# Kernel tuning notes

Hardware: AMD Instinct MI355X
Metric: run time of the kernel (lower is better)

The kernel has to match this reference:

```python
import jax, jax.numpy as jnp
import numpy as np

D_MODEL = 1024
NUM_HEADS = 16
NUM_KV_HEADS = 4
HEAD_DIM = D_MODEL // NUM_HEADS  # 64
THETA = 10000.0
MAX_SEQ_LEN = 4096


def _rope_tables(max_seq_len, d_k, theta):
    k_vec = jnp.arange(0, d_k, 2, dtype=jnp.float32) / d_k
    freq = 1.0 / (theta ** k_vec)                       # (d_k/2,)
    ang = jnp.arange(max_seq_len, dtype=jnp.float32)[:, None] * freq[None, :]
    return jnp.cos(ang), jnp.sin(ang)                   # each (max_seq_len, d_k/2)


def _apply_rope(x, pos, cos_table, sin_table):
    # x: (b, h, l, d), pos: (b, l)
    cos = cos_table[pos][:, None, :, :]                 # (b, 1, l, d/2)
    sin = sin_table[pos][:, None, :, :]
    even, odd = x[..., 0::2], x[..., 1::2]
    r1 = even * cos - odd * sin
    r2 = even * sin + odd * cos
    return jnp.stack([r1, r2], axis=-1).reshape(x.shape)  # interleave back


def setup_inputs() -> dict:
    key = jax.random.key(0)
    ks = jax.random.split(key, 6)
    B, L, D = 1, 4096, D_MODEL
    std = (2.0 / (D + D)) ** 0.5
    std_kv = (2.0 / (D + HEAD_DIM * NUM_KV_HEADS)) ** 0.5
    x = jax.random.normal(ks[0], (B, L, D), dtype=jnp.float32)
    Wq = jax.random.normal(ks[1], (D, D), dtype=jnp.float32) * std
    Wk = jax.random.normal(ks[2], (HEAD_DIM * NUM_KV_HEADS, D), dtype=jnp.float32) * std_kv
    Wv = jax.random.normal(ks[3], (HEAD_DIM * NUM_KV_HEADS, D), dtype=jnp.float32) * std_kv
    Wo = jax.random.normal(ks[4], (D, D), dtype=jnp.float32) * std
    token_positions = jnp.broadcast_to(jnp.arange(L, dtype=jnp.int32), (B, L))
    return {"x": x, "Wq": Wq, "Wk": Wk, "Wv": Wv, "Wo": Wo,
            "token_positions": token_positions}


def reference(x, Wq, Wk, Wv, Wo, token_positions):
    B, L, D = x.shape
    H, Hkv, Dh = NUM_HEADS, NUM_KV_HEADS, HEAD_DIM
    n_rep = H // Hkv
    cos_t, sin_t = _rope_tables(MAX_SEQ_LEN, Dh, THETA)

    q = (x @ Wq.T).reshape(B, L, H, Dh).transpose(0, 2, 1, 3)      # b h l d
    k = (x @ Wk.T).reshape(B, L, Hkv, Dh).transpose(0, 2, 1, 3)    # b g l d
    v = (x @ Wv.T).reshape(B, L, Hkv, Dh).transpose(0, 2, 1, 3)

    q = _apply_rope(q, token_positions, cos_t, sin_t)
    k = _apply_rope(k, token_positions, cos_t, sin_t)

    # GQA: group query heads by kv head
    qg = q.reshape(B, Hkv, n_rep, L, Dh)
    scores = jnp.einsum('bgrqd,bgkd->bgrqk', qg, k) / jnp.sqrt(jnp.float32(Dh))
    causal = jnp.tril(jnp.ones((L, L), dtype=bool))
    scores = jnp.where(causal, scores, -jnp.inf)
    weights = jax.nn.softmax(scores, axis=-1)
    out = jnp.einsum('bgrqk,bgkd->bgrqd', weights, v)              # b g r q d
    out = out.reshape(B, H, L, Dh).transpose(0, 2, 1, 3).reshape(B, L, D)
    return out @ Wo.T
```

## Files before the change

### kernel.cpp

```cpp
#include <hip/hip_runtime.h>
#include <hip/hip_bf16.h>
#include <math.h>

typedef __bf16 bf16;
typedef __bf16 v8bf __attribute__((ext_vector_type(8)));
typedef __bf16 v4bf __attribute__((ext_vector_type(4)));
typedef float f32x4 __attribute__((ext_vector_type(4)));

#define L_SEQ 4096
#define DMODEL 1024
#define NHEADS 16
#define DH 64
#define NEG_BIG (-1e30f)
#define LN1E4_64 0.14391156f

__global__ void convert_all(const float* __restrict__ x, const float* __restrict__ wq,
                            const float* __restrict__ wk, const float* __restrict__ wv,
                            const float* __restrict__ wo,
                            bf16* __restrict__ xb, bf16* __restrict__ wqkvb,
                            bf16* __restrict__ wob) {
    int i = (blockIdx.x * 256 + threadIdx.x) * 4;
    const float* src;
    bf16* dst;
    if (i < 4194304)      { src = x  + i;             dst = xb    + i; }
    else if (i < 5242880) { src = wq + (i - 4194304); dst = wqkvb + (i - 4194304); }
    else if (i < 5505024) { src = wk + (i - 5242880); dst = wqkvb + 1048576 + (i - 5242880); }
    else if (i < 5767168) { src = wv + (i - 5505024); dst = wqkvb + 1310720 + (i - 5505024); }
    else                  { src = wo + (i - 5767168); dst = wob   + (i - 5767168); }
    f32x4 v = *(const f32x4*)src;
    v4bf r;
#pragma unroll
    for (int j = 0; j < 4; j++) r[j] = (bf16)v[j];
    *(v4bf*)dst = r;
}

__global__ __launch_bounds__(512) void gemm_qkv(const bf16* __restrict__ A,
                                                const bf16* __restrict__ W,
                                                bf16* __restrict__ Qb,
                                                bf16* __restrict__ Kb,
                                                bf16* __restrict__ Vtg,
                                                const int* __restrict__ tp) {
    __shared__ bf16 As[128][68];
    __shared__ bf16 Bs[128][68];
    const int K = 1024;
    const int tid = threadIdx.x;
    const int w = tid >> 6, lane = tid & 63;
    const int quad = lane >> 4, l16 = lane & 15;
    const int wm = (w & 1) * 64, wn = (w >> 1) * 32;
    const int bm = blockIdx.y * 128, bn = blockIdx.x * 128;

    f32x4 acc[4][2];
#pragma unroll
    for (int mf = 0; mf < 4; mf++)
#pragma unroll
        for (int nf = 0; nf < 2; nf++) acc[mf][nf] = (f32x4){0.f, 0.f, 0.f, 0.f};

    const int sr = tid >> 2;
    const int scb = (tid & 3) * 16;

    v8bf pa0, pa1, pb0, pb1;
    {
        const bf16* ap = &A[(size_t)(bm + sr) * K + scb];
        const bf16* bp = &W[(size_t)(bn + sr) * K + scb];
        pa0 = *(const v8bf*)ap; pa1 = *(const v8bf*)(ap + 8);
        pb0 = *(const v8bf*)bp; pb1 = *(const v8bf*)(bp + 8);
        *(v8bf*)&As[sr][scb] = pa0; *(v8bf*)&As[sr][scb + 8] = pa1;
        *(v8bf*)&Bs[sr][scb] = pb0; *(v8bf*)&Bs[sr][scb + 8] = pb1;
    }

    for (int kt = 0; kt < K; kt += 64) {
        __syncthreads();
        const bool more = (kt + 64) < K;
        if (more) {
            const bf16* ap = &A[(size_t)(bm + sr) * K + kt + 64 + scb];
            const bf16* bp = &W[(size_t)(bn + sr) * K + kt + 64 + scb];
            pa0 = *(const v8bf*)ap; pa1 = *(const v8bf*)(ap + 8);
            pb0 = *(const v8bf*)bp; pb1 = *(const v8bf*)(bp + 8);
        }
#pragma unroll
        for (int kf = 0; kf < 2; kf++) {
            v8bf a[4], b[2];
#pragma unroll
            for (int mf = 0; mf < 4; mf++) a[mf] = *(v8bf*)&As[wm + mf * 16 + l16][kf * 32 + quad * 8];
#pragma unroll
            for (int nf = 0; nf < 2; nf++) b[nf] = *(v8bf*)&Bs[wn + nf * 16 + l16][kf * 32 + quad * 8];
#pragma unroll
            for (int mf = 0; mf < 4; mf++)
#pragma unroll
                for (int nf = 0; nf < 2; nf++)
                    acc[mf][nf] = __builtin_amdgcn_mfma_f32_16x16x32_bf16(a[mf], b[nf], acc[mf][nf], 0, 0, 0);
        }
        __syncthreads();
        if (more) {
            *(v8bf*)&As[sr][scb] = pa0; *(v8bf*)&As[sr][scb + 8] = pa1;
            *(v8bf*)&Bs[sr][scb] = pb0; *(v8bf*)&Bs[sr][scb + 8] = pb1;
        }
    }

    if (bn < 1024) {
#pragma unroll
        for (int mf = 0; mf < 4; mf++) {
            int pos_[4];
#pragma unroll
            for (int r = 0; r < 4; r++) pos_[r] = tp[bm + wm + mf * 16 + quad * 4 + r];
#pragma unroll
            for (int nf = 0; nf < 2; nf++) {
                const int col = bn + wn + nf * 16 + l16;
                float fr = __expf(-(float)((col & 63) & ~1) * LN1E4_64);
#pragma unroll
                for (int r = 0; r < 4; r++) {
                    float v = acc[mf][nf][r];
                    float sn, cs;
                    __sincosf((float)pos_[r] * fr, &sn, &cs);
                    float p = __shfl_xor(v, 1);
                    float res = (l16 & 1) ? (p * sn + v * cs) : (v * cs - p * sn);
                    int row = bm + wm + mf * 16 + quad * 4 + r;
                    Qb[(size_t)row * DMODEL + col] = (bf16)res;
                }
            }
        }
    } else if (bn < 1280) {
#pragma unroll
        for (int mf = 0; mf < 4; mf++) {
            int pos_[4];
#pragma unroll
            for (int r = 0; r < 4; r++) pos_[r] = tp[bm + wm + mf * 16 + quad * 4 + r];
#pragma unroll
            for (int nf = 0; nf < 2; nf++) {
                const int kcol = bn - 1024 + wn + nf * 16 + l16;
                float fr = __expf(-(float)((kcol & 63) & ~1) * LN1E4_64);
#pragma unroll
                for (int r = 0; r < 4; r++) {
                    float v = acc[mf][nf][r];
                    float sn, cs;
                    __sincosf((float)pos_[r] * fr, &sn, &cs);
                    float p = __shfl_xor(v, 1);
                    float res = (l16 & 1) ? (p * sn + v * cs) : (v * cs - p * sn);
                    int row = bm + wm + mf * 16 + quad * 4 + r;
                    Kb[(size_t)row * 256 + kcol] = (bf16)res;
                }
            }
        }
    } else {
#pragma unroll
        for (int mf = 0; mf < 4; mf++)
#pragma unroll
            for (int nf = 0; nf < 2; nf++) {
                v4bf pk;
#pragma unroll
                for (int r = 0; r < 4; r++) pk[r] = (bf16)acc[mf][nf][r];
                int vcol = bn - 1280 + wn + nf * 16 + l16;
                int row = bm + wm + mf * 16 + quad * 4;
                *(v4bf*)&Vtg[(size_t)vcol * L_SEQ + row] = pk;
            }
    }
}

__global__ __launch_bounds__(512) void gemm_out(const bf16* __restrict__ A,
                                                const bf16* __restrict__ W,
                                                float* __restrict__ C) {
    __shared__ bf16 As[128][68];
    __shared__ bf16 Bs[128][68];
    const int K = 1024, N = 1024;
    const int tid = threadIdx.x;
    const int w = tid >> 6, lane = tid & 63;
    const int quad = lane >> 4, l16 = lane & 15;
    const int wm = (w & 1) * 64, wn = (w >> 1) * 32;
    const int bm = blockIdx.y * 128, bn = blockIdx.x * 128;

    f32x4 acc[4][2];
#pragma unroll
    for (int mf = 0; mf < 4; mf++)
#pragma unroll
        for (int nf = 0; nf < 2; nf++) acc[mf][nf] = (f32x4){0.f, 0.f, 0.f, 0.f};

    const int sr = tid >> 2;
    const int scb = (tid & 3) * 16;

    v8bf pa0, pa1, pb0, pb1;
    {
        const bf16* ap = &A[(size_t)(bm + sr) * K + scb];
        const bf16* bp = &W[(size_t)(bn + sr) * K + scb];
        pa0 = *(const v8bf*)ap; pa1 = *(const v8bf*)(ap + 8);
        pb0 = *(const v8bf*)bp; pb1 = *(const v8bf*)(bp + 8);
        *(v8bf*)&As[sr][scb] = pa0; *(v8bf*)&As[sr][scb + 8] = pa1;
        *(v8bf*)&Bs[sr][scb] = pb0; *(v8bf*)&Bs[sr][scb + 8] = pb1;
    }

    for (int kt = 0; kt < K; kt += 64) {
        __syncthreads();
        const bool more = (kt + 64) < K;
        if (more) {
            const bf16* ap = &A[(size_t)(bm + sr) * K + kt + 64 + scb];
            const bf16* bp = &W[(size_t)(bn + sr) * K + kt + 64 + scb];
            pa0 = *(const v8bf*)ap; pa1 = *(const v8bf*)(ap + 8);
            pb0 = *(const v8bf*)bp; pb1 = *(const v8bf*)(bp + 8);
        }
#pragma unroll
        for (int kf = 0; kf < 2; kf++) {
            v8bf a[4], b[2];
#pragma unroll
            for (int mf = 0; mf < 4; mf++) a[mf] = *(v8bf*)&As[wm + mf * 16 + l16][kf * 32 + quad * 8];
#pragma unroll
            for (int nf = 0; nf < 2; nf++) b[nf] = *(v8bf*)&Bs[wn + nf * 16 + l16][kf * 32 + quad * 8];
#pragma unroll
            for (int mf = 0; mf < 4; mf++)
#pragma unroll
                for (int nf = 0; nf < 2; nf++)
                    acc[mf][nf] = __builtin_amdgcn_mfma_f32_16x16x32_bf16(a[mf], b[nf], acc[mf][nf], 0, 0, 0);
        }
        __syncthreads();
        if (more) {
            *(v8bf*)&As[sr][scb] = pa0; *(v8bf*)&As[sr][scb + 8] = pa1;
            *(v8bf*)&Bs[sr][scb] = pb0; *(v8bf*)&Bs[sr][scb + 8] = pb1;
        }
    }
#pragma unroll
    for (int mf = 0; mf < 4; mf++)
#pragma unroll
        for (int nf = 0; nf < 2; nf++)
#pragma unroll
            for (int r = 0; r < 4; r++) {
                int row = bm + wm + mf * 16 + quad * 4 + r;
                int col = bn + wn + nf * 16 + l16;
                C[(size_t)row * N + col] = acc[mf][nf][r];
            }
}

__global__ __launch_bounds__(256, 2) void flash5(const bf16* __restrict__ Q,
                                                 const bf16* __restrict__ Kb,
                                                 const bf16* __restrict__ Vtg,
                                                 bf16* __restrict__ O0,
                                                 bf16* __restrict__ O1,
                                                 float* __restrict__ ML) {
    __shared__ bf16 Ks[128][68];
    __shared__ bf16 Vt[64][132];
    __shared__ bf16 Ps[128][68];
    const int h = blockIdx.y, kvh = h >> 2;
    const int bx = blockIdx.x;
    const int tid = threadIdx.x;
    const int w = tid >> 6, lane = tid & 63;
    const int quad = lane >> 4, l16 = lane & 15;
    const int krow = tid >> 1, kcb = (tid & 1) * 32;
    const int vr = tid >> 2, vcb = (tid & 3) * 32;
    const float scl = 0.125f;

    for (int p = 0; p < 2; p++) {
        const int qb = p ? (31 - bx) : bx;
        const int T = qb + 1;
        const int k0 = p ? ((T + 1) >> 1) : 0;
        const int k1 = p ? T : ((T + 1) >> 1);
        bf16* Op = p ? O1 : O0;
        float* mlp = ML + (size_t)(p * NHEADS + h) * L_SEQ * 2;

        if (k0 >= k1) {
            for (int i = tid; i < 128 * 64; i += 256) {
                int rr = i >> 6, cc = i & 63;
                Op[(size_t)(qb * 128 + rr) * DMODEL + h * DH + cc] = (bf16)0.f;
            }
            if (tid < 128) {
                mlp[(qb * 128 + tid) * 2 + 0] = NEG_BIG;
                mlp[(qb * 128 + tid) * 2 + 1] = 0.f;
            }
            continue;
        }

        v8bf qf[2][2];
#pragma unroll
        for (int mf = 0; mf < 2; mf++)
#pragma unroll
            for (int kf = 0; kf < 2; kf++)
                qf[mf][kf] = *(const v8bf*)&Q[(size_t)(qb * 128 + w * 32 + mf * 16 + l16) * DMODEL
                                              + h * DH + kf * 32 + quad * 8];

        f32x4 oacc[2][4];
#pragma unroll
        for (int mf = 0; mf < 2; mf++)
#pragma unroll
            for (int d = 0; d < 4; d++) oacc[mf][d] = (f32x4){0.f, 0.f, 0.f, 0.f};
        float m_i[2][4], l_i[2][4];
#pragma unroll
        for (int mf = 0; mf < 2; mf++)
#pragma unroll
            for (int r = 0; r < 4; r++) { m_i[mf][r] = NEG_BIG; l_i[mf][r] = 0.f; }

        v8bf kreg[4], vreg[4];
        {
            const bf16* ks = &Kb[(size_t)(k0 * 128 + krow) * 256 + kvh * DH + kcb];
            const bf16* vs = &Vtg[(size_t)(kvh * DH + vr) * L_SEQ + k0 * 128 + vcb];
#pragma unroll
            for (int u = 0; u < 4; u++) { kreg[u] = *(const v8bf*)&ks[8 * u]; vreg[u] = *(const v8bf*)&vs[8 * u]; }
            __syncthreads();
#pragma unroll
            for (int u = 0; u < 4; u++) { *(v8bf*)&Ks[krow][kcb + 8 * u] = kreg[u]; *(v8bf*)&Vt[vr][vcb + 8 * u] = vreg[u]; }
        }

        for (int kb = k0; kb < k1; kb++) {
            __syncthreads();
            if (kb + 1 < k1) {
                const bf16* ks = &Kb[(size_t)((kb + 1) * 128 + krow) * 256 + kvh * DH + kcb];
                const bf16* vs = &Vtg[(size_t)(kvh * DH + vr) * L_SEQ + (kb + 1) * 128 + vcb];
#pragma unroll
                for (int u = 0; u < 4; u++) { kreg[u] = *(const v8bf*)&ks[8 * u]; vreg[u] = *(const v8bf*)&vs[8 * u]; }
            }

            f32x4 s[2][8];
#pragma unroll
            for (int n = 0; n < 8; n++) {
                v8bf b0 = *(v8bf*)&Ks[n * 16 + l16][quad * 8];
                v8bf b1 = *(v8bf*)&Ks[n * 16 + l16][32 + quad * 8];
#pragma unroll
                for (int mf = 0; mf < 2; mf++) {
                    s[mf][n] = (f32x4){0.f, 0.f, 0.f, 0.f};
                    s[mf][n] = __builtin_amdgcn_mfma_f32_16x16x32_bf16(qf[mf][0], b0, s[mf][n], 0, 0, 0);
                    s[mf][n] = __builtin_amdgcn_mfma_f32_16x16x32_bf16(qf[mf][1], b1, s[mf][n], 0, 0, 0);
                }
            }

            if (kb == qb) {
#pragma unroll
                for (int mf = 0; mf < 2; mf++) {
                    int rbase = qb * 128 + w * 32 + mf * 16 + quad * 4;
#pragma unroll
                    for (int n = 0; n < 8; n++) {
                        int colg = kb * 128 + n * 16 + l16;
#pragma unroll
                        for (int r = 0; r < 4; r++)
                            s[mf][n][r] = (colg <= rbase + r) ? s[mf][n][r] * scl : NEG_BIG;
                    }
                }
            } else {
#pragma unroll
                for (int mf = 0; mf < 2; mf++)
#pragma unroll
                    for (int n = 0; n < 8; n++)
#pragma unroll
                        for (int r = 0; r < 4; r++) s[mf][n][r] *= scl;
            }

            float mx[2][4];
#pragma unroll
            for (int mf = 0; mf < 2; mf++)
#pragma unroll
                for (int r = 0; r < 4; r++) {
                    float m0 = s[mf][0][r];
#pragma unroll
                    for (int n = 1; n < 8; n++) m0 = fmaxf(m0, s[mf][n][r]);
                    mx[mf][r] = m0;
                }
#pragma unroll
            for (int off = 1; off < 16; off <<= 1)
#pragma unroll
                for (int mf = 0; mf < 2; mf++)
#pragma unroll
                    for (int r = 0; r < 4; r++)
                        mx[mf][r] = fmaxf(mx[mf][r], __shfl_xor(mx[mf][r], off));

            float alpha[2][4], mnew[2][4], rs[2][4];
#pragma unroll
            for (int mf = 0; mf < 2; mf++)
#pragma unroll
                for (int r = 0; r < 4; r++) {
                    mnew[mf][r]  = fmaxf(m_i[mf][r], mx[mf][r]);
                    alpha[mf][r] = __expf(m_i[mf][r] - mnew[mf][r]);
                    rs[mf][r] = 0.f;
                }
#pragma unroll
            for (int mf = 0; mf < 2; mf++)
#pragma unroll
                for (int n = 0; n < 8; n++)
#pragma unroll
                    for (int r = 0; r < 4; r++) {
                        float pv = __expf(s[mf][n][r] - mnew[mf][r]);
                        s[mf][n][r] = pv;
                        rs[mf][r] += pv;
                    }
#pragma unroll
            for (int off = 1; off < 16; off <<= 1)
#pragma unroll
                for (int mf = 0; mf < 2; mf++)
#pragma unroll
                    for (int r = 0; r < 4; r++) rs[mf][r] += __shfl_xor(rs[mf][r], off);
#pragma unroll
            for (int mf = 0; mf < 2; mf++)
#pragma unroll
                for (int r = 0; r < 4; r++) {
                    l_i[mf][r] = l_i[mf][r] * alpha[mf][r] + rs[mf][r];
                    m_i[mf][r] = mnew[mf][r];
                }
#pragma unroll
            for (int mf = 0; mf < 2; mf++)
#pragma unroll
                for (int d = 0; d < 4; d++)
#pragma unroll
                    for (int r = 0; r < 4; r++) oacc[mf][d][r] *= alpha[mf][r];

#pragma unroll
            for (int half = 0; half < 2; half++) {
#pragma unroll
                for (int mf = 0; mf < 2; mf++)
#pragma unroll
                    for (int n = 0; n < 4; n++)
#pragma unroll
                        for (int r = 0; r < 4; r++)
                            Ps[w * 32 + mf * 16 + quad * 4 + r][n * 16 + l16] =
                                (bf16)s[mf][half * 4 + n][r];
#pragma unroll
                for (int kf = 0; kf < 2; kf++) {
#pragma unroll
                    for (int mf = 0; mf < 2; mf++) {
                        v8bf pa = *(v8bf*)&Ps[w * 32 + mf * 16 + l16][kf * 32 + quad * 8];
#pragma unroll
                        for (int d = 0; d < 4; d++) {
                            v8bf vb = *(v8bf*)&Vt[d * 16 + l16][half * 64 + kf * 32 + quad * 8];
                            oacc[mf][d] = __builtin_amdgcn_mfma_f32_16x16x32_bf16(pa, vb, oacc[mf][d], 0, 0, 0);
                        }
                    }
                }
            }

            __syncthreads();
            if (kb + 1 < k1) {
#pragma unroll
                for (int u = 0; u < 4; u++) { *(v8bf*)&Ks[krow][kcb + 8 * u] = kreg[u]; *(v8bf*)&Vt[vr][vcb + 8 * u] = vreg[u]; }
            }
        }

#pragma unroll
        for (int mf = 0; mf < 2; mf++)
#pragma unroll
            for (int d = 0; d < 4; d++)
#pragma unroll
                for (int r = 0; r < 4; r++) {
                    int row = qb * 128 + w * 32 + mf * 16 + quad * 4 + r;
                    Op[(size_t)row * DMODEL + h * DH + d * 16 + l16] = (bf16)oacc[mf][d][r];
                }
        if (l16 == 0) {
#pragma unroll
            for (int mf = 0; mf < 2; mf++)
#pragma unroll
                for (int r = 0; r < 4; r++) {
                    int row = qb * 128 + w * 32 + mf * 16 + quad * 4 + r;
                    mlp[row * 2 + 0] = m_i[mf][r];
                    mlp[row * 2 + 1] = l_i[mf][r];
                }
        }
    }
}

__global__ void combine(const bf16* __restrict__ O0, const bf16* __restrict__ O1,
                        const float* __restrict__ ML, bf16* __restrict__ Attn) {
    int gid = blockIdx.x * 256 + threadIdx.x;
    int row = gid >> 8;
    int cg = (gid & 255) * 4;
    int h = cg >> 6;
    const float* ml0 = ML + ((size_t)h * L_SEQ + row) * 2;
    const float* ml1 = ML + ((size_t)(NHEADS + h) * L_SEQ + row) * 2;
    float m0 = ml0[0], l0 = ml0[1], m1 = ml1[0], l1 = ml1[1];
    float m = fmaxf(m0, m1);
    float a0 = __expf(m0 - m), a1 = __expf(m1 - m);
    float inv = 1.f / (a0 * l0 + a1 * l1);
    v4bf o0 = *(const v4bf*)&O0[(size_t)row * DMODEL + cg];
    v4bf o1 = *(const v4bf*)&O1[(size_t)row * DMODEL + cg];
    v4bf res;
#pragma unroll
    for (int j = 0; j < 4; j++)
        res[j] = (bf16)((a0 * (float)o0[j] + a1 * (float)o1[j]) * inv);
    *(v4bf*)&Attn[(size_t)row * DMODEL + cg] = res;
}

extern "C" void kernel_launch(void* const* d_in, const int* in_sizes, int n_in,
                              void* d_out, int out_size, void* d_ws, size_t ws_size,
                              hipStream_t stream) {
    const float* x  = (const float*)d_in[0];
    const float* Wq = (const float*)d_in[1];
    const float* Wk = (const float*)d_in[2];
    const float* Wv = (const float*)d_in[3];
    const float* Wo = (const float*)d_in[4];
    const int*   tp = (const int*)d_in[5];
    float* out = (float*)d_out;

    bf16*  xb    = (bf16*)d_ws;
    bf16*  wqkvb = xb    + 4194304;
    bf16*  wob   = wqkvb + 1572864;
    bf16*  Qb    = wob   + 1048576;
    bf16*  Kb    = Qb    + 4194304;
    bf16*  Vtg   = Kb    + 1048576;
    float* MLf   = (float*)(Vtg + 1048576);
    bf16*  Attn  = xb;
    bf16*  O0    = (bf16*)d_out;
    bf16*  O1    = O0 + 4194304;

    convert_all<<<6656, 256, 0, stream>>>(x, Wq, Wk, Wv, Wo, xb, wqkvb, wob);
    gemm_qkv<<<dim3(12, 32), 512, 0, stream>>>(xb, wqkvb, Qb, Kb, Vtg, tp);
    flash5<<<dim3(32, NHEADS), 256, 0, stream>>>(Qb, Kb, Vtg, O0, O1, MLf);
    combine<<<4096, 256, 0, stream>>>(O0, O1, MLf, Attn);
    gemm_out<<<dim3(8, 32), 512, 0, stream>>>(Attn, wob, out);
}
```

Baseline: 226.2 us.

## Split attention KV range four ways, fold softmax scale into Q, share LDS

The flash kernel now splits each query block's causal key range into four partitions instead of two, launching 64x16 blocks that each handle two partitions chosen to balance work. A four-way combine kernel merges the partial outputs. The softmax scale and log2(e) are folded into Q at the RoPE epilogue so the inner loop can use exp2 without a per-score multiply. K and P tiles share one LDS buffer, guarded by an extra barrier, and launch bounds are raised to 4 blocks per SM. The aim is more parallelism and occupancy, paid for with extra partial-output traffic, a larger combine step and one more sync per iteration.

```diff
diff --git a/kernel.cpp b/kernel.cpp
--- a/kernel.cpp
+++ b/kernel.cpp
@@ -13,6 +13,9 @@
 #define DH 64
 #define NEG_BIG (-1e30f)
 #define LN1E4_64 0.14391156f
+#define QSCALE 0.18033688f
+
+__device__ inline float fast_exp2(float x) { return __builtin_amdgcn_exp2f(x); }
 
 __global__ void convert_all(const float* __restrict__ x, const float* __restrict__ wq,
                             const float* __restrict__ wk, const float* __restrict__ wv,
@@ -115,7 +118,7 @@
                     float p = __shfl_xor(v, 1);
                     float res = (l16 & 1) ? (p * sn + v * cs) : (v * cs - p * sn);
                     int row = bm + wm + mf * 16 + quad * 4 + r;
-                    Qb[(size_t)row * DMODEL + col] = (bf16)res;
+                    Qb[(size_t)row * DMODEL + col] = (bf16)(res * QSCALE);
                 }
             }
         }
@@ -227,15 +230,16 @@
             }
 }
 
-__global__ __launch_bounds__(256, 2) void flash5(const bf16* __restrict__ Q,
+__global__ __launch_bounds__(256, 4) void flash6(const bf16* __restrict__ Q,
                                                  const bf16* __restrict__ Kb,
                                                  const bf16* __restrict__ Vtg,
                                                  bf16* __restrict__ O0,
                                                  bf16* __restrict__ O1,
+                                                 bf16* __restrict__ O2,
+                                                 bf16* __restrict__ O3,
                                                  float* __restrict__ ML) {
-    __shared__ bf16 Ks[128][68];
+    __shared__ bf16 KsPs[128][68];
     __shared__ bf16 Vt[64][132];
-    __shared__ bf16 Ps[128][68];
     const int h = blockIdx.y, kvh = h >> 2;
     const int bx = blockIdx.x;
     const int tid = threadIdx.x;
@@ -243,19 +247,22 @@
     const int quad = lane >> 4, l16 = lane & 15;
     const int krow = tid >> 1, kcb = (tid & 1) * 32;
     const int vr = tid >> 2, vcb = (tid & 3) * 32;
-    const float scl = 0.125f;
+    bf16* const Ops[4] = {O0, O1, O2, O3};
+
+    const int q0 = bx >> 1, i0 = bx & 1;
 
     for (int p = 0; p < 2; p++) {
-        const int qb = p ? (31 - bx) : bx;
+        const int qb = p ? (31 - q0) : q0;
+        const int j  = p ? (3 - i0) : i0;
         const int T = qb + 1;
-        const int k0 = p ? ((T + 1) >> 1) : 0;
-        const int k1 = p ? T : ((T + 1) >> 1);
-        bf16* Op = p ? O1 : O0;
-        float* mlp = ML + (size_t)(p * NHEADS + h) * L_SEQ * 2;
+        const int k0 = (j * T) >> 2;
+        const int k1 = ((j + 1) * T) >> 2;
+        bf16* Op = Ops[j];
+        float* mlp = ML + (size_t)(j * NHEADS + h) * L_SEQ * 2;
 
         if (k0 >= k1) {
-            for (int i = tid; i < 128 * 64; i += 256) {
-                int rr = i >> 6, cc = i & 63;
+            for (int idx = tid; idx < 128 * 64; idx += 256) {
+                int rr = idx >> 6, cc = idx & 63;
                 Op[(size_t)(qb * 128 + rr) * DMODEL + h * DH + cc] = (bf16)0.f;
             }
             if (tid < 128) {
@@ -292,7 +299,7 @@
             for (int u = 0; u < 4; u++) { kreg[u] = *(const v8bf*)&ks[8 * u]; vreg[u] = *(const v8bf*)&vs[8 * u]; }
             __syncthreads();
 #pragma unroll
-            for (int u = 0; u < 4; u++) { *(v8bf*)&Ks[krow][kcb + 8 * u] = kreg[u]; *(v8bf*)&Vt[vr][vcb + 8 * u] = vreg[u]; }
+            for (int u = 0; u < 4; u++) { *(v8bf*)&KsPs[krow][kcb + 8 * u] = kreg[u]; *(v8bf*)&Vt[vr][vcb + 8 * u] = vreg[u]; }
         }
 
         for (int kb = k0; kb < k1; kb++) {
@@ -307,8 +314,8 @@
             f32x4 s[2][8];
 #pragma unroll
             for (int n = 0; n < 8; n++) {
-                v8bf b0 = *(v8bf*)&Ks[n * 16 + l16][quad * 8];
-                v8bf b1 = *(v8bf*)&Ks[n * 16 + l16][32 + quad * 8];
+                v8bf b0 = *(v8bf*)&KsPs[n * 16 + l16][quad * 8];
+                v8bf b1 = *(v8bf*)&KsPs[n * 16 + l16][32 + quad * 8];
 #pragma unroll
                 for (int mf = 0; mf < 2; mf++) {
                     s[mf][n] = (f32x4){0.f, 0.f, 0.f, 0.f};
@@ -326,16 +333,9 @@
                         int colg = kb * 128 + n * 16 + l16;
 #pragma unroll
                         for (int r = 0; r < 4; r++)
-                            s[mf][n][r] = (colg <= rbase + r) ? s[mf][n][r] * scl : NEG_BIG;
+                            s[mf][n][r] = (colg <= rbase + r) ? s[mf][n][r] : NEG_BIG;
                     }
                 }
-            } else {
-#pragma unroll
-                for (int mf = 0; mf < 2; mf++)
-#pragma unroll
-                    for (int n = 0; n < 8; n++)
-#pragma unroll
-                        for (int r = 0; r < 4; r++) s[mf][n][r] *= scl;
             }
 
             float mx[2][4];
@@ -362,7 +362,7 @@
 #pragma unroll
                 for (int r = 0; r < 4; r++) {
                     mnew[mf][r]  = fmaxf(m_i[mf][r], mx[mf][r]);
-                    alpha[mf][r] = __expf(m_i[mf][r] - mnew[mf][r]);
+                    alpha[mf][r] = fast_exp2(m_i[mf][r] - mnew[mf][r]);
                     rs[mf][r] = 0.f;
                 }
 #pragma unroll
@@ -371,7 +371,7 @@
                 for (int n = 0; n < 8; n++)
 #pragma unroll
                     for (int r = 0; r < 4; r++) {
-                        float pv = __expf(s[mf][n][r] - mnew[mf][r]);
+                        float pv = fast_exp2(s[mf][n][r] - mnew[mf][r]);
                         s[mf][n][r] = pv;
                         rs[mf][r] += pv;
                     }
@@ -395,6 +395,8 @@
 #pragma unroll
                     for (int r = 0; r < 4; r++) oacc[mf][d][r] *= alpha[mf][r];
 
+            __syncthreads();
+
 #pragma unroll
             for (int half = 0; half < 2; half++) {
 #pragma unroll
@@ -403,13 +405,13 @@
                     for (int n = 0; n < 4; n++)
 #pragma unroll
                         for (int r = 0; r < 4; r++)
-                            Ps[w * 32 + mf * 16 + quad * 4 + r][n * 16 + l16] =
+                            KsPs[w * 32 + mf * 16 + quad * 4 + r][n * 16 + l16] =
                                 (bf16)s[mf][half * 4 + n][r];
 #pragma unroll
                 for (int kf = 0; kf < 2; kf++) {
 #pragma unroll
                     for (int mf = 0; mf < 2; mf++) {
-                        v8bf pa = *(v8bf*)&Ps[w * 32 + mf * 16 + l16][kf * 32 + quad * 8];
+                        v8bf pa = *(v8bf*)&KsPs[w * 32 + mf * 16 + l16][kf * 32 + quad * 8];
 #pragma unroll
                         for (int d = 0; d < 4; d++) {
                             v8bf vb = *(v8bf*)&Vt[d * 16 + l16][half * 64 + kf * 32 + quad * 8];
@@ -422,7 +424,7 @@
             __syncthreads();
             if (kb + 1 < k1) {
 #pragma unroll
-                for (int u = 0; u < 4; u++) { *(v8bf*)&Ks[krow][kcb + 8 * u] = kreg[u]; *(v8bf*)&Vt[vr][vcb + 8 * u] = vreg[u]; }
+                for (int u = 0; u < 4; u++) { *(v8bf*)&KsPs[krow][kcb + 8 * u] = kreg[u]; *(v8bf*)&Vt[vr][vcb + 8 * u] = vreg[u]; }
             }
         }
 
@@ -448,24 +450,33 @@
     }
 }
 
-__global__ void combine(const bf16* __restrict__ O0, const bf16* __restrict__ O1,
-                        const float* __restrict__ ML, bf16* __restrict__ Attn) {
+__global__ void combine4(const bf16* __restrict__ O0, const bf16* __restrict__ O1,
+                         const bf16* __restrict__ O2, const bf16* __restrict__ O3,
+                         const float* __restrict__ ML, bf16* __restrict__ Attn) {
     int gid = blockIdx.x * 256 + threadIdx.x;
     int row = gid >> 8;
     int cg = (gid & 255) * 4;
     int h = cg >> 6;
-    const float* ml0 = ML + ((size_t)h * L_SEQ + row) * 2;
-    const float* ml1 = ML + ((size_t)(NHEADS + h) * L_SEQ + row) * 2;
-    float m0 = ml0[0], l0 = ml0[1], m1 = ml1[0], l1 = ml1[1];
-    float m = fmaxf(m0, m1);
-    float a0 = __expf(m0 - m), a1 = __expf(m1 - m);
-    float inv = 1.f / (a0 * l0 + a1 * l1);
+    float m[4], l[4];
+#pragma unroll
+    for (int j = 0; j < 4; j++) {
+        const float* ml = ML + (((size_t)(j * NHEADS + h) * L_SEQ) + row) * 2;
+        m[j] = ml[0]; l[j] = ml[1];
+    }
+    float mmax = fmaxf(fmaxf(m[0], m[1]), fmaxf(m[2], m[3]));
+    float a[4], denom = 0.f;
+#pragma unroll
+    for (int j = 0; j < 4; j++) { a[j] = fast_exp2(m[j] - mmax); denom += a[j] * l[j]; }
+    float inv = 1.f / denom;
     v4bf o0 = *(const v4bf*)&O0[(size_t)row * DMODEL + cg];
     v4bf o1 = *(const v4bf*)&O1[(size_t)row * DMODEL + cg];
+    v4bf o2 = *(const v4bf*)&O2[(size_t)row * DMODEL + cg];
+    v4bf o3 = *(const v4bf*)&O3[(size_t)row * DMODEL + cg];
     v4bf res;
 #pragma unroll
-    for (int j = 0; j < 4; j++)
-        res[j] = (bf16)((a0 * (float)o0[j] + a1 * (float)o1[j]) * inv);
+    for (int jj = 0; jj < 4; jj++)
+        res[jj] = (bf16)((a[0] * (float)o0[jj] + a[1] * (float)o1[jj] +
+                          a[2] * (float)o2[jj] + a[3] * (float)o3[jj]) * inv);
     *(v4bf*)&Attn[(size_t)row * DMODEL + cg] = res;
 }
 
@@ -486,14 +497,16 @@
     bf16*  Qb    = wob   + 1048576;
     bf16*  Kb    = Qb    + 4194304;
     bf16*  Vtg   = Kb    + 1048576;
-    float* MLf   = (float*)(Vtg + 1048576);
+    bf16*  O2    = Vtg   + 1048576;
+    bf16*  O3    = O2    + 4194304;
+    float* MLf   = (float*)(O3 + 4194304);
     bf16*  Attn  = xb;
     bf16*  O0    = (bf16*)d_out;
     bf16*  O1    = O0 + 4194304;
 
     convert_all<<<6656, 256, 0, stream>>>(x, Wq, Wk, Wv, Wo, xb, wqkvb, wob);
     gemm_qkv<<<dim3(12, 32), 512, 0, stream>>>(xb, wqkvb, Qb, Kb, Vtg, tp);
-    flash5<<<dim3(32, NHEADS), 256, 0, stream>>>(Qb, Kb, Vtg, O0, O1, MLf);
-    combine<<<4096, 256, 0, stream>>>(O0, O1, MLf, Attn);
+    flash6<<<dim3(64, NHEADS), 256, 0, stream>>>(Qb, Kb, Vtg, O0, O1, O2, O3, MLf);
+    combine4<<<4096, 256, 0, stream>>>(O0, O1, O2, O3, MLf, Attn);
     gemm_out<<<dim3(8, 32), 512, 0, stream>>>(Attn, wob, out);
 }
```

Result: slower. 397.3 us (+75.6%).
